# Performance work log

Measured on AMD Instinct MI355X. Metric: run time of the kernel, lower is better.

The kernel has to match this reference:

```python
import jax, jax.numpy as jnp
import numpy as np

B, T, D = 4, 2048, 1024
C_BIAS = 0.0  # init kwarg c
LN_EPS = 1e-5


def setup_inputs() -> dict:
    key = jax.random.key(0)
    ks = jax.random.split(key, 8)
    s = 1.0 / np.sqrt(D)
    return {
        "x": jax.random.normal(ks[0], (B, T, D), dtype=jnp.float32),
        "l": jax.random.randint(ks[1], (B,), 1, T + 1),  # lengths in [1, T]
        "Wq": jax.random.normal(ks[2], (D, D), dtype=jnp.float32) * s,
        "Wk": jax.random.normal(ks[3], (D, D), dtype=jnp.float32) * s,
        "Wv": jax.random.normal(ks[4], (D, D), dtype=jnp.float32) * s,
        "Wo": jax.random.normal(ks[5], (D, D), dtype=jnp.float32) * s,
        "bo": jnp.zeros((D,), dtype=jnp.float32),
        "gamma": jnp.ones((D,), dtype=jnp.float32),
        "beta": jnp.zeros((D,), dtype=jnp.float32),
    }


def reference(x, l, Wq, Wk, Wv, Wo, bo, gamma, beta):
    # LayerNorm over last dim
    mu = jnp.mean(x, axis=-1, keepdims=True)
    var = jnp.mean(jnp.square(x - mu), axis=-1, keepdims=True)
    x_norm = (x - mu) * jax.lax.rsqrt(var + LN_EPS) * gamma + beta

    # QKV projections (torch Linear: y = x @ W.T, no bias)
    q = jnp.einsum("btd,ed->bte", x_norm, Wq)
    k = jnp.einsum("btd,ed->bte", x_norm, Wk)
    v = jnp.einsum("btd,ed->bte", x_norm, Wv)

    scale = 1.0 / jnp.sqrt(jnp.float32(D))
    scores = C_BIAS + jnp.einsum("bid,bjd->bij", q, k) * scale  # [B,T,T]

    # Mask is applied along the ROW (dim 1) axis, and softmax is over dim 1
    # (faithful to the original: mask.unsqueeze(2) + Softmax(dim=1)).
    valid_rows = jnp.arange(T)[None, :] < l[:, None]  # [B,T]
    scores = jnp.where(valid_rows[:, :, None], scores, -jnp.inf)
    attn = jax.nn.softmax(scores, axis=1)  # normalize over rows

    y = x + jnp.einsum("bij,bjd->bid", attn, v)
    out = jax.nn.relu(jnp.einsum("btd,ed->bte", y, Wo) + bo)
    return out
```

## Files before the change

kernel.cpp:

```cpp
#include <hip/hip_runtime.h>
#include <hip/hip_fp16.h>

typedef unsigned short u16;
typedef __attribute__((ext_vector_type(8))) short bf16x8;
typedef __attribute__((ext_vector_type(4))) float f32x4;

#define T_SEQ 2048
#define DIM 1024
#define NB 4
#define NCH 8

__device__ __forceinline__ u16 f2bf(float f) {
  union { float f; unsigned u; } c; c.f = f;
  unsigned r = c.u + 0x7fffu + ((c.u >> 16) & 1u);
  return (u16)(r >> 16);
}

__device__ __forceinline__ void gload_lds16(const void* g, void* l) {
  __builtin_amdgcn_global_load_lds((const __attribute__((address_space(1))) void*)g,
                                   (__attribute__((address_space(3))) void*)l, 16, 0, 0);
}

#define SBAR() asm volatile("s_barrier" ::: "memory")
#define WVL(n) asm volatile("s_waitcnt vmcnt(" n ") lgkmcnt(0)" ::: "memory")

__global__ __launch_bounds__(256) void ln_kernel(const float* __restrict__ x,
                                                 const float* __restrict__ gamma,
                                                 const float* __restrict__ beta,
                                                 u16* __restrict__ xn) {
  const int row = blockIdx.x;
  const int tid = threadIdx.x;
  const float4 v = *(const float4*)(x + (size_t)row * DIM + tid * 4);
  float s  = v.x + v.y + v.z + v.w;
  float ss = v.x * v.x + v.y * v.y + v.z * v.z + v.w * v.w;
#pragma unroll
  for (int o = 32; o > 0; o >>= 1) { s += __shfl_down(s, o); ss += __shfl_down(ss, o); }
  __shared__ float rs[4], rss[4];
  const int wid = tid >> 6, lane = tid & 63;
  if (lane == 0) { rs[wid] = s; rss[wid] = ss; }
  __syncthreads();
  s  = rs[0] + rs[1] + rs[2] + rs[3];
  ss = rss[0] + rss[1] + rss[2] + rss[3];
  const float mu = s * (1.f / DIM);
  const float var = ss * (1.f / DIM) - mu * mu;
  const float rstd = rsqrtf(var + 1e-5f);
  const float4 g  = *(const float4*)(gamma + tid * 4);
  const float4 be = *(const float4*)(beta + tid * 4);
  ushort4 o;
  o.x = f2bf((v.x - mu) * rstd * g.x + be.x);
  o.y = f2bf((v.y - mu) * rstd * g.y + be.y);
  o.z = f2bf((v.z - mu) * rstd * g.z + be.z);
  o.w = f2bf((v.w - mu) * rstd * g.w + be.w);
  *(ushort4*)(xn + (size_t)row * DIM + tid * 4) = o;
}

__global__ __launch_bounds__(256) void wcvt4(const float* __restrict__ wq,
                                             const float* __restrict__ wk,
                                             const float* __restrict__ wv,
                                             const float* __restrict__ wo,
                                             u16* __restrict__ dqk,
                                             u16* __restrict__ dv,
                                             u16* __restrict__ dw) {
  const int sel = blockIdx.x >> 10;
  const size_t t = (size_t)(blockIdx.x & 1023) * 256 + threadIdx.x;
  const float* w = (sel == 0) ? wq : (sel == 1) ? wk : (sel == 2) ? wv : wo;
  u16* d = (sel == 0) ? dqk : (sel == 1) ? (dqk + 1048576) : (sel == 2) ? dv : dw;
  const float4 v = *(const float4*)(w + t * 4);
  ushort4 u; u.x = f2bf(v.x); u.y = f2bf(v.y); u.z = f2bf(v.z); u.w = f2bf(v.w);
  *(ushort4*)(d + t * 4) = u;
}

template <int EPI, int BM, int MSK>
__global__ __launch_bounds__(512, 2) void gemm_bt(
    const u16* __restrict__ A, const u16* __restrict__ B, void* __restrict__ Cv,
    int K, int lda, int ldb, int ldc,
    long sA, long sB, long sC,
    const float* __restrict__ aux, long sAux, float scale,
    const int* __restrict__ lptr, float* __restrict__ mpQ, float* __restrict__ zpQ) {
  constexpr int MI = BM / 32;
  __shared__ __align__(16) u16 As[4][BM * 32];
  __shared__ __align__(16) u16 Bs[4][256 * 32];
  const int bz = blockIdx.z;
  const u16* Ab = A + (size_t)bz * sA;
  const u16* Bb = B + (size_t)bz * sB;

  const int nb = gridDim.x * gridDim.y;
  int bid = blockIdx.y * gridDim.x + blockIdx.x;
  bid = (bid & 7) * (nb >> 3) + (bid >> 3);
  const int gx = gridDim.x;
  const int tileN = (bid % gx) * 256;
  const int tileM = (bid / gx) * BM;

  const int t = threadIdx.x;

  if constexpr (MSK == 1) {
    if (tileM >= lptr[bz]) return;
  }
  if constexpr (MSK == 3) {
    if (((tileM & (T_SEQ - 1)) >= lptr[tileM >> 11]) && tileN < DIM) return;
  }
  if constexpr (MSK == 2) {
    if (tileM >= lptr[bz]) {
      const float* xb = aux + (size_t)bz * sAux;
      u16* yo = (u16*)Cv + (size_t)bz * sC;
      for (int e = t; e < (BM * 256) / 8; e += 512) {
        const int row = tileM + (e >> 5);
        const int col = tileN + ((e & 31) << 3);
        const float4 v0 = *(const float4*)(xb + (size_t)row * ldc + col);
        const float4 v1 = *(const float4*)(xb + (size_t)row * ldc + col + 4);
        ushort4 o0; o0.x = f2bf(v0.x); o0.y = f2bf(v0.y); o0.z = f2bf(v0.z); o0.w = f2bf(v0.w);
        ushort4 o1; o1.x = f2bf(v1.x); o1.y = f2bf(v1.y); o1.z = f2bf(v1.z); o1.w = f2bf(v1.w);
        *(ushort4*)(yo + (size_t)row * ldc + col) = o0;
        *(ushort4*)(yo + (size_t)row * ldc + col + 4) = o1;
      }
      return;
    }
  }

  const int lane = t & 63;
  const int wid = t >> 6;
  const int wm = wid >> 2, wn = wid & 3;

  const int srow = t >> 2;
  const int qsw = (((t & 3) ^ (srow & 3) ^ ((srow >> 2) & 3))) * 8;
  const size_t aoff0 = (size_t)(tileM + srow) * lda + qsw;
  const size_t aoff1 = (size_t)(tileM + 128 + srow) * lda + qsw;
  const size_t boff0 = (size_t)(tileN + srow) * ldb + qsw;
  const size_t boff1 = (size_t)(tileN + 128 + srow) * ldb + qsw;

  const int frow = lane & 15;
  const int kg = lane >> 4;
  const int ckk = ((kg ^ (lane & 3) ^ ((lane >> 2) & 3))) * 8;

  f32x4 acc[MI][4] = {};
  const int NT = K >> 5;

#pragma unroll
  for (int p = 0; p < 3; ++p) {
    const size_t kp = (size_t)p << 5;
    gload_lds16(Ab + aoff0 + kp, &As[p][t * 8]);
    gload_lds16(Bb + boff0 + kp, &Bs[p][t * 8]);
    if constexpr (BM == 256) gload_lds16(Ab + aoff1 + kp, &As[p][4096 + t * 8]);
    gload_lds16(Bb + boff1 + kp, &Bs[p][4096 + t * 8]);
  }
  if constexpr (BM == 256) { asm volatile("s_waitcnt vmcnt(8)" ::: "memory"); }
  else                     { asm volatile("s_waitcnt vmcnt(6)" ::: "memory"); }
  SBAR();

  for (int tau = 0; tau < NT; ++tau) {
    const int cur = tau & 3;
    const int tgt = (tau + 3) & 3;
    const bool st = (tau + 3 < NT);
    const size_t k0 = (size_t)(tau + 3) << 5;

    bf16x8 af[4], bf[4];
#pragma unroll
    for (int j = 0; j < 4; ++j)
      bf[j] = *(const bf16x8*)&Bs[cur][(wn * 64 + j * 16 + frow) * 32 + ckk];
#pragma unroll
    for (int i = 0; i < 4; ++i)
      af[i] = *(const bf16x8*)&As[cur][(wm * (BM / 2) + i * 16 + frow) * 32 + ckk];
    if (st) {
      gload_lds16(Ab + aoff0 + k0, &As[tgt][t * 8]);
      gload_lds16(Bb + boff0 + k0, &Bs[tgt][t * 8]);
      if constexpr (BM == 128) gload_lds16(Bb + boff1 + k0, &Bs[tgt][4096 + t * 8]);
    }
    if constexpr (BM == 128) {
      if (tau < NT - 3) WVL("6"); else if (tau == NT - 3) WVL("3"); else WVL("0");
    }
    SBAR();
    __builtin_amdgcn_s_setprio(1);
#pragma unroll
    for (int i = 0; i < 4; ++i)
#pragma unroll
      for (int j = 0; j < 4; ++j)
        acc[i][j] = __builtin_amdgcn_mfma_f32_16x16x32_bf16(af[i], bf[j], acc[i][j], 0, 0, 0);
    __builtin_amdgcn_s_setprio(0);

    if constexpr (BM == 256) {
      bf16x8 af2[4];
#pragma unroll
      for (int i = 0; i < 4; ++i)
        af2[i] = *(const bf16x8*)&As[cur][(wm * 128 + (4 + i) * 16 + frow) * 32 + ckk];
      if (st) {
        gload_lds16(Ab + aoff1 + k0, &As[tgt][4096 + t * 8]);
        gload_lds16(Bb + boff1 + k0, &Bs[tgt][4096 + t * 8]);
      }
      if (tau < NT - 3) WVL("8"); else if (tau == NT - 3) WVL("4"); else WVL("0");
      SBAR();
      __builtin_amdgcn_s_setprio(1);
#pragma unroll
      for (int i = 0; i < 4; ++i)
#pragma unroll
        for (int j = 0; j < 4; ++j)
          acc[4 + i][j] = __builtin_amdgcn_mfma_f32_16x16x32_bf16(af2[i], bf[j], acc[4 + i][j], 0, 0, 0);
      __builtin_amdgcn_s_setprio(0);
    }
  }

  const int r0 = tileM + wm * (BM / 2) + (kg << 2);
  const int c0 = tileN + wn * 64 + frow;
#pragma unroll
  for (int i = 0; i < MI; ++i)
#pragma unroll
    for (int j = 0; j < 4; ++j)
#pragma unroll
      for (int r = 0; r < 4; ++r) {
        const int row = r0 + i * 16 + r, col = c0 + j * 16;
        const size_t idx = (size_t)row * ldc + col;
        float v = acc[i][j][r];
        if constexpr (EPI == 0) {
          ((u16*)Cv + (size_t)bz * sC)[idx] = f2bf(v);
        } else if constexpr (EPI == 1) {
          ((__half*)Cv + (size_t)bz * sC)[idx] = __float2half(v * scale);
        } else if constexpr (EPI == 2) {
          v += (aux + (size_t)bz * sAux)[idx];
          ((u16*)Cv + (size_t)bz * sC)[idx] = f2bf(v);
        } else {
          v += aux[col];
          ((float*)Cv + (size_t)bz * sC)[idx] = fmaxf(v, 0.f);
        }
      }

  if constexpr (EPI == 1) {
    const int L = lptr[bz];
    __shared__ float2 red[2][4][4][16];
    float Ms[4], Zs[4];
#pragma unroll
    for (int j = 0; j < 4; ++j) {
      float mj = -3e38f;
#pragma unroll
      for (int i = 0; i < MI; ++i)
#pragma unroll
        for (int r = 0; r < 4; ++r) {
          const int row = r0 + i * 16 + r;
          if (row < L) mj = fmaxf(mj, acc[i][j][r] * scale);
        }
      mj = fmaxf(mj, __shfl_xor(mj, 16, 64));
      mj = fmaxf(mj, __shfl_xor(mj, 32, 64));
      float zj = 0.f;
#pragma unroll
      for (int i = 0; i < MI; ++i)
#pragma unroll
        for (int r = 0; r < 4; ++r) {
          const int row = r0 + i * 16 + r;
          if (row < L) zj += __expf(acc[i][j][r] * scale - mj);
        }
      zj += __shfl_xor(zj, 16, 64);
      zj += __shfl_xor(zj, 32, 64);
      Ms[j] = mj; Zs[j] = zj;
    }
    if (lane < 16) {
#pragma unroll
      for (int j = 0; j < 4; ++j) red[wm][wn][j][frow] = make_float2(Ms[j], Zs[j]);
    }
    __syncthreads();
    if (wm == 0 && lane < 16) {
#pragma unroll
      for (int j = 0; j < 4; ++j) {
        const float2 a = red[0][wn][j][frow];
        const float2 b = red[1][wn][j][frow];
        const float M = fmaxf(a.x, b.x);
        const float Z = a.y * __expf(a.x - M) + b.y * __expf(b.x - M);
        const int col = tileN + wn * 64 + j * 16 + frow;
        const size_t o = ((size_t)(tileM >> 8) * NB + bz) * T_SEQ + col;
        mpQ[o] = M; zpQ[o] = Z;
      }
    }
  }
}

__global__ __launch_bounds__(256) void colreduce_comb(const float* __restrict__ mp,
                                                      const float* __restrict__ zp,
                                                      const int* __restrict__ l,
                                                      float* __restrict__ m,
                                                      float* __restrict__ rz) {
  const int b = blockIdx.y;
  const int j = blockIdx.x * 256 + threadIdx.x;
  const int L = l[b];
  float M = -3e38f, Z = 0.f;
  for (int c = 0; c < NCH && (c << 8) < L; ++c) {
    const size_t o = ((size_t)c * NB + b) * T_SEQ + j;
    const float mc = mp[o], zc = zp[o];
    const float nm = fmaxf(M, mc);
    Z = Z * __expf(M - nm) + zc * __expf(mc - nm);
    M = nm;
  }
  m[b * T_SEQ + j] = M;
  rz[b * T_SEQ + j] = 1.f / Z;
}

__global__ __launch_bounds__(256) void pbuild(const __half* __restrict__ S,
                                              const int* __restrict__ l,
                                              const float* __restrict__ m,
                                              const float* __restrict__ rz,
                                              u16* __restrict__ P) {
  const int b = blockIdx.x >> 11;
  const int i = blockIdx.x & (T_SEQ - 1);
  const int L = l[b];
  if (i >= ((L + 127) & ~127)) return;
  const int j0 = threadIdx.x * 8;
  const size_t off = ((size_t)blockIdx.x << 11) + j0;
  ushort4 o0, o1;
  if (i < L) {
    const __half* sp = S + off;
    const float* mp = m + b * T_SEQ + j0;
    const float* zp = rz + b * T_SEQ + j0;
    u16 tmp[8];
#pragma unroll
    for (int t = 0; t < 8; ++t)
      tmp[t] = f2bf(__expf(__half2float(sp[t]) - mp[t]) * zp[t]);
    o0 = make_ushort4(tmp[0], tmp[1], tmp[2], tmp[3]);
    o1 = make_ushort4(tmp[4], tmp[5], tmp[6], tmp[7]);
  } else {
    o0 = make_ushort4(0, 0, 0, 0);
    o1 = make_ushort4(0, 0, 0, 0);
  }
  *(ushort4*)(P + off) = o0;
  *(ushort4*)(P + off + 4) = o1;
}

extern "C" void kernel_launch(void* const* d_in, const int* in_sizes, int n_in,
                              void* d_out, int out_size, void* d_ws, size_t ws_size,
                              hipStream_t stream) {
  (void)in_sizes; (void)n_in; (void)out_size; (void)ws_size;
  const float* x     = (const float*)d_in[0];
  const int*   l     = (const int*)d_in[1];
  const float* Wq    = (const float*)d_in[2];
  const float* Wk    = (const float*)d_in[3];
  const float* Wv    = (const float*)d_in[4];
  const float* Wo    = (const float*)d_in[5];
  const float* bo    = (const float*)d_in[6];
  const float* gamma = (const float*)d_in[7];
  const float* beta  = (const float*)d_in[8];

  char* ws = (char*)d_ws;
  const size_t MiB = 1024 * 1024;
  u16* xn   = (u16*)(ws);
  u16* wqkb = (u16*)(ws + 16 * MiB);
  u16* wvb  = (u16*)(ws + 20 * MiB);
  u16* wob  = (u16*)(ws + 22 * MiB);
  u16* QKb  = (u16*)(ws + 24 * MiB);
  u16* Vt   = (u16*)(ws + 56 * MiB);
  float* mpart = (float*)(ws + 20 * MiB);
  float* zpart = (float*)(ws + 20 * MiB + 512 * 1024);
  float* mb  = (float*)(ws + 72 * MiB);
  float* rzb = (float*)(ws + 72 * MiB + 32 * 1024);
  u16* Pb = QKb;
  u16* yb = xn;
  __half* S = (__half*)d_out;
  float* outp = (float*)d_out;

  const long TD = (long)T_SEQ * DIM, TT = (long)T_SEQ * T_SEQ;
  const long TQK = (long)T_SEQ * 2048;

  ln_kernel<<<NB * T_SEQ, 256, 0, stream>>>(x, gamma, beta, xn);
  wcvt4<<<4096, 256, 0, stream>>>(Wq, Wk, Wv, Wo, wqkb, wvb, wob);

  gemm_bt<0, 256, 3><<<dim3(8, 32, 1), 512, 0, stream>>>(
      xn, wqkb, QKb, DIM, DIM, DIM, 2048, 0, 0, 0, nullptr, 0, 0.f,
      l, nullptr, nullptr);
  gemm_bt<0, 128, 0><<<dim3(32, 8, 1), 512, 0, stream>>>(
      wvb, xn, Vt, DIM, DIM, DIM, 8192, 0, 0, 0, nullptr, 0, 0.f,
      nullptr, nullptr, nullptr);
  gemm_bt<1, 256, 1><<<dim3(8, 8, NB), 512, 0, stream>>>(
      QKb, QKb + 1024, S, DIM, 2048, 2048, T_SEQ, TQK, TQK, TT, nullptr, 0, 0.03125f,
      l, mpart, zpart);
  colreduce_comb<<<dim3(T_SEQ / 256, NB), 256, 0, stream>>>(mpart, zpart, l, mb, rzb);
  pbuild<<<NB * T_SEQ, 256, 0, stream>>>(S, l, mb, rzb, Pb);
  gemm_bt<2, 128, 2><<<dim3(4, 16, NB), 512, 0, stream>>>(
      Pb, Vt, yb, T_SEQ, T_SEQ, 8192, DIM, TT, 2048, TD, x, TD, 0.f,
      l, nullptr, nullptr);
  gemm_bt<3, 128, 0><<<dim3(4, 64, 1), 512, 0, stream>>>(
      yb, wob, outp, DIM, DIM, DIM, DIM, 0, 0, 0, bo, 0, 0.f,
      nullptr, nullptr, nullptr);
}
```

Measured before the change: 208.4 us.

## Add 256x256 GEMM kernel with K=64 double-buffered, finer-grained staged pipeline

Adds a dedicated 256x256-tile GEMM kernel (gemm8) for the QK projection and the QK^T score GEMM. It stages K in 64-wide steps across two double-buffered halves and interleaves half-tile LDS loads, global-to-LDS prefetches and MFMA blocks with barriers between them. The aim is to hide memory latency better than the previous 4-stage, 32-wide scheme. The remaining GEMMs keep a simplified BM=128-only kernel. It adds more barriers per step and a more fragile hand-counted vmcnt schedule.

```diff
diff --git a/kernel.cpp b/kernel.cpp
--- a/kernel.cpp
+++ b/kernel.cpp
@@ -23,6 +23,7 @@
 
 #define SBAR() asm volatile("s_barrier" ::: "memory")
 #define WVL(n) asm volatile("s_waitcnt vmcnt(" n ") lgkmcnt(0)" ::: "memory")
+#define VMC(n) asm volatile("s_waitcnt vmcnt(" n ")" ::: "memory")
 
 __global__ __launch_bounds__(256) void ln_kernel(const float* __restrict__ x,
                                                  const float* __restrict__ gamma,
@@ -70,16 +71,14 @@
   *(ushort4*)(d + t * 4) = u;
 }
 
-template <int EPI, int BM, int MSK>
-__global__ __launch_bounds__(512, 2) void gemm_bt(
+template <int EPI, int MSK>
+__global__ __launch_bounds__(512, 2) void gemm8(
     const u16* __restrict__ A, const u16* __restrict__ B, void* __restrict__ Cv,
     int K, int lda, int ldb, int ldc,
-    long sA, long sB, long sC,
-    const float* __restrict__ aux, long sAux, float scale,
+    long sA, long sB, long sC, float scale,
     const int* __restrict__ lptr, float* __restrict__ mpQ, float* __restrict__ zpQ) {
-  constexpr int MI = BM / 32;
-  __shared__ __align__(16) u16 As[4][BM * 32];
-  __shared__ __align__(16) u16 Bs[4][256 * 32];
+  __shared__ __align__(16) u16 As[2][2][8192];
+  __shared__ __align__(16) u16 Bs[2][2][8192];
   const int bz = blockIdx.z;
   const u16* Ab = A + (size_t)bz * sA;
   const u16* Bb = B + (size_t)bz * sB;
@@ -89,9 +88,7 @@
   bid = (bid & 7) * (nb >> 3) + (bid >> 3);
   const int gx = gridDim.x;
   const int tileN = (bid % gx) * 256;
-  const int tileM = (bid / gx) * BM;
-
-  const int t = threadIdx.x;
+  const int tileM = (bid / gx) * 256;
 
   if constexpr (MSK == 1) {
     if (tileM >= lptr[bz]) return;
@@ -99,11 +96,181 @@
   if constexpr (MSK == 3) {
     if (((tileM & (T_SEQ - 1)) >= lptr[tileM >> 11]) && tileN < DIM) return;
   }
+
+  const int t = threadIdx.x;
+  const int lane = t & 63;
+  const int wid = t >> 6;
+  const int wm = wid >> 2, wn = wid & 3;
+
+  const int srow = wid * 32 + (lane >> 2);
+  const int schk = ((t & 3) ^ (srow & 3) ^ ((srow >> 2) & 3)) * 8;
+  const size_t aof = (size_t)(tileM + srow) * lda + schk;
+  const size_t bof = (size_t)(tileN + srow) * ldb + schk;
+  const size_t a16 = 16 * (size_t)lda, b16 = 16 * (size_t)ldb;
+  const int dst0 = wid * 1024 + lane * 8;
+
+  const int frow = lane & 15, kg = lane >> 4;
+  const int rsw = (kg ^ (frow & 3) ^ ((frow >> 2) & 3)) * 8;
+  const int arow = wm * 128 + frow;
+  const int brow = wn * 64 + frow;
+
+#define STG_A(bf, kk, tg) do { \
+    const size_t _s = aof + (size_t)(tg) * 64 + (kk) * 32; \
+    gload_lds16(Ab + _s, &As[bf][kk][dst0]); \
+    gload_lds16(Ab + _s + a16, &As[bf][kk][dst0 + 512]); } while (0)
+#define STG_B(bf, kk, tg) do { \
+    const size_t _s = bof + (size_t)(tg) * 64 + (kk) * 32; \
+    gload_lds16(Bb + _s, &Bs[bf][kk][dst0]); \
+    gload_lds16(Bb + _s + b16, &Bs[bf][kk][dst0 + 512]); } while (0)
+#define LDA4(bf, kk, h, AF) do { \
+    _Pragma("unroll") for (int _i = 0; _i < 4; ++_i) \
+      AF[_i] = *(const bf16x8*)&As[bf][kk][(arow + (h) * 64 + _i * 16) * 32 + rsw]; } while (0)
+#define LDB4(bf, kk, BF) do { \
+    _Pragma("unroll") for (int _j = 0; _j < 4; ++_j) \
+      BF[_j] = *(const bf16x8*)&Bs[bf][kk][(brow + _j * 16) * 32 + rsw]; } while (0)
+#define MFM(h, AF, BF) do { __builtin_amdgcn_s_setprio(1); \
+    _Pragma("unroll") for (int _i = 0; _i < 4; ++_i) \
+      _Pragma("unroll") for (int _j = 0; _j < 4; ++_j) \
+        acc[(h) * 4 + _i][_j] = __builtin_amdgcn_mfma_f32_16x16x32_bf16( \
+            AF[_i], BF[_j], acc[(h) * 4 + _i][_j], 0, 0, 0); \
+    __builtin_amdgcn_s_setprio(0); } while (0)
+
+  f32x4 acc[8][4] = {};
+  const int NT = K >> 6;
+
+  STG_B(0, 0, 0); STG_A(0, 0, 0);
+  STG_B(0, 1, 0); STG_A(0, 1, 0);
+  STG_B(1, 0, 1); STG_A(1, 0, 1);
+  VMC("4");
+  SBAR();
+
+  for (int tt = 0; tt < NT; tt += 2) {
+    const bool st = (tt + 2 < NT);
+    bf16x8 af[4], bq0[4], bq1[4];
+    LDA4(0, 0, 0, af); LDB4(0, 0, bq0);
+    STG_B(1, 1, tt + 1);
+    SBAR(); MFM(0, af, bq0);
+    LDA4(0, 0, 1, af);
+    STG_A(1, 1, tt + 1);
+    SBAR(); MFM(1, af, bq0);
+    LDA4(0, 1, 0, af); LDB4(0, 1, bq1);
+    if (st) STG_B(0, 0, tt + 2);
+    SBAR(); MFM(0, af, bq1);
+    LDA4(0, 1, 1, af);
+    if (st) { STG_A(0, 0, tt + 2); VMC("4"); } else { VMC("0"); }
+    SBAR(); MFM(1, af, bq1);
+    LDA4(1, 0, 0, af); LDB4(1, 0, bq0);
+    if (st) STG_B(0, 1, tt + 2);
+    SBAR(); MFM(0, af, bq0);
+    LDA4(1, 0, 1, af);
+    if (st) STG_A(0, 1, tt + 2);
+    SBAR(); MFM(1, af, bq0);
+    LDA4(1, 1, 0, af); LDB4(1, 1, bq1);
+    if (st) STG_B(1, 0, tt + 3);
+    SBAR(); MFM(0, af, bq1);
+    LDA4(1, 1, 1, af);
+    if (st) { STG_A(1, 0, tt + 3); VMC("2"); } else { VMC("0"); }
+    SBAR(); MFM(1, af, bq1);
+  }
+#undef STG_A
+#undef STG_B
+#undef LDA4
+#undef LDB4
+#undef MFM
+
+  const int r0 = tileM + wm * 128 + (kg << 2);
+  const int c0 = tileN + wn * 64 + frow;
+#pragma unroll
+  for (int i = 0; i < 8; ++i)
+#pragma unroll
+    for (int j = 0; j < 4; ++j)
+#pragma unroll
+      for (int r = 0; r < 4; ++r) {
+        const int row = r0 + i * 16 + r, col = c0 + j * 16;
+        const size_t idx = (size_t)row * ldc + col;
+        const float v = acc[i][j][r];
+        if constexpr (EPI == 0) {
+          ((u16*)Cv + (size_t)bz * sC)[idx] = f2bf(v);
+        } else {
+          ((__half*)Cv + (size_t)bz * sC)[idx] = __float2half(v * scale);
+        }
+      }
+
+  if constexpr (EPI == 1) {
+    const int L = lptr[bz];
+    __shared__ float2 red[2][4][4][16];
+    float Ms[4], Zs[4];
+#pragma unroll
+    for (int j = 0; j < 4; ++j) {
+      float mj = -3e38f;
+#pragma unroll
+      for (int i = 0; i < 8; ++i)
+#pragma unroll
+        for (int r = 0; r < 4; ++r) {
+          const int row = r0 + i * 16 + r;
+          if (row < L) mj = fmaxf(mj, acc[i][j][r] * scale);
+        }
+      mj = fmaxf(mj, __shfl_xor(mj, 16, 64));
+      mj = fmaxf(mj, __shfl_xor(mj, 32, 64));
+      float zj = 0.f;
+#pragma unroll
+      for (int i = 0; i < 8; ++i)
+#pragma unroll
+        for (int r = 0; r < 4; ++r) {
+          const int row = r0 + i * 16 + r;
+          if (row < L) zj += __expf(acc[i][j][r] * scale - mj);
+        }
+      zj += __shfl_xor(zj, 16, 64);
+      zj += __shfl_xor(zj, 32, 64);
+      Ms[j] = mj; Zs[j] = zj;
+    }
+    if (lane < 16) {
+#pragma unroll
+      for (int j = 0; j < 4; ++j) red[wm][wn][j][frow] = make_float2(Ms[j], Zs[j]);
+    }
+    __syncthreads();
+    if (wm == 0 && lane < 16) {
+#pragma unroll
+      for (int j = 0; j < 4; ++j) {
+        const float2 a = red[0][wn][j][frow];
+        const float2 b = red[1][wn][j][frow];
+        const float M = fmaxf(a.x, b.x);
+        const float Z = a.y * __expf(a.x - M) + b.y * __expf(b.x - M);
+        const int col = tileN + wn * 64 + j * 16 + frow;
+        const size_t o = ((size_t)(tileM >> 8) * NB + bz) * T_SEQ + col;
+        mpQ[o] = M; zpQ[o] = Z;
+      }
+    }
+  }
+}
+
+template <int EPI, int MSK>
+__global__ __launch_bounds__(512, 2) void gemm_bt(
+    const u16* __restrict__ A, const u16* __restrict__ B, void* __restrict__ Cv,
+    int K, int lda, int ldb, int ldc,
+    long sA, long sB, long sC,
+    const float* __restrict__ aux, long sAux,
+    const int* __restrict__ lptr) {
+  __shared__ __align__(16) u16 As[4][128 * 32];
+  __shared__ __align__(16) u16 Bs[4][256 * 32];
+  const int bz = blockIdx.z;
+  const u16* Ab = A + (size_t)bz * sA;
+  const u16* Bb = B + (size_t)bz * sB;
+
+  const int nb = gridDim.x * gridDim.y;
+  int bid = blockIdx.y * gridDim.x + blockIdx.x;
+  bid = (bid & 7) * (nb >> 3) + (bid >> 3);
+  const int gx = gridDim.x;
+  const int tileN = (bid % gx) * 256;
+  const int tileM = (bid / gx) * 128;
+
+  const int t = threadIdx.x;
+
   if constexpr (MSK == 2) {
     if (tileM >= lptr[bz]) {
       const float* xb = aux + (size_t)bz * sAux;
       u16* yo = (u16*)Cv + (size_t)bz * sC;
-      for (int e = t; e < (BM * 256) / 8; e += 512) {
+      for (int e = t; e < (128 * 256) / 8; e += 512) {
         const int row = tileM + (e >> 5);
         const int col = tileN + ((e & 31) << 3);
         const float4 v0 = *(const float4*)(xb + (size_t)row * ldc + col);
@@ -124,7 +291,6 @@
   const int srow = t >> 2;
   const int qsw = (((t & 3) ^ (srow & 3) ^ ((srow >> 2) & 3))) * 8;
   const size_t aoff0 = (size_t)(tileM + srow) * lda + qsw;
-  const size_t aoff1 = (size_t)(tileM + 128 + srow) * lda + qsw;
   const size_t boff0 = (size_t)(tileN + srow) * ldb + qsw;
   const size_t boff1 = (size_t)(tileN + 128 + srow) * ldb + qsw;
 
@@ -132,7 +298,7 @@
   const int kg = lane >> 4;
   const int ckk = ((kg ^ (lane & 3) ^ ((lane >> 2) & 3))) * 8;
 
-  f32x4 acc[MI][4] = {};
+  f32x4 acc[4][4] = {};
   const int NT = K >> 5;
 
 #pragma unroll
@@ -140,11 +306,9 @@
     const size_t kp = (size_t)p << 5;
     gload_lds16(Ab + aoff0 + kp, &As[p][t * 8]);
     gload_lds16(Bb + boff0 + kp, &Bs[p][t * 8]);
-    if constexpr (BM == 256) gload_lds16(Ab + aoff1 + kp, &As[p][4096 + t * 8]);
     gload_lds16(Bb + boff1 + kp, &Bs[p][4096 + t * 8]);
   }
-  if constexpr (BM == 256) { asm volatile("s_waitcnt vmcnt(8)" ::: "memory"); }
-  else                     { asm volatile("s_waitcnt vmcnt(6)" ::: "memory"); }
+  VMC("6");
   SBAR();
 
   for (int tau = 0; tau < NT; ++tau) {
@@ -159,15 +323,13 @@
       bf[j] = *(const bf16x8*)&Bs[cur][(wn * 64 + j * 16 + frow) * 32 + ckk];
 #pragma unroll
     for (int i = 0; i < 4; ++i)
-      af[i] = *(const bf16x8*)&As[cur][(wm * (BM / 2) + i * 16 + frow) * 32 + ckk];
+      af[i] = *(const bf16x8*)&As[cur][(wm * 64 + i * 16 + frow) * 32 + ckk];
     if (st) {
       gload_lds16(Ab + aoff0 + k0, &As[tgt][t * 8]);
       gload_lds16(Bb + boff0 + k0, &Bs[tgt][t * 8]);
-      if constexpr (BM == 128) gload_lds16(Bb + boff1 + k0, &Bs[tgt][4096 + t * 8]);
+      gload_lds16(Bb + boff1 + k0, &Bs[tgt][4096 + t * 8]);
     }
-    if constexpr (BM == 128) {
-      if (tau < NT - 3) WVL("6"); else if (tau == NT - 3) WVL("3"); else WVL("0");
-    }
+    if (tau < NT - 3) WVL("6"); else if (tau == NT - 3) WVL("3"); else WVL("0");
     SBAR();
     __builtin_amdgcn_s_setprio(1);
 #pragma unroll
@@ -176,32 +338,12 @@
       for (int j = 0; j < 4; ++j)
         acc[i][j] = __builtin_amdgcn_mfma_f32_16x16x32_bf16(af[i], bf[j], acc[i][j], 0, 0, 0);
     __builtin_amdgcn_s_setprio(0);
-
-    if constexpr (BM == 256) {
-      bf16x8 af2[4];
-#pragma unroll
-      for (int i = 0; i < 4; ++i)
-        af2[i] = *(const bf16x8*)&As[cur][(wm * 128 + (4 + i) * 16 + frow) * 32 + ckk];
-      if (st) {
-        gload_lds16(Ab + aoff1 + k0, &As[tgt][4096 + t * 8]);
-        gload_lds16(Bb + boff1 + k0, &Bs[tgt][4096 + t * 8]);
-      }
-      if (tau < NT - 3) WVL("8"); else if (tau == NT - 3) WVL("4"); else WVL("0");
-      SBAR();
-      __builtin_amdgcn_s_setprio(1);
-#pragma unroll
-      for (int i = 0; i < 4; ++i)
-#pragma unroll
-        for (int j = 0; j < 4; ++j)
-          acc[4 + i][j] = __builtin_amdgcn_mfma_f32_16x16x32_bf16(af2[i], bf[j], acc[4 + i][j], 0, 0, 0);
-      __builtin_amdgcn_s_setprio(0);
-    }
-  }
-
-  const int r0 = tileM + wm * (BM / 2) + (kg << 2);
+  }
+
+  const int r0 = tileM + wm * 64 + (kg << 2);
   const int c0 = tileN + wn * 64 + frow;
 #pragma unroll
-  for (int i = 0; i < MI; ++i)
+  for (int i = 0; i < 4; ++i)
 #pragma unroll
     for (int j = 0; j < 4; ++j)
 #pragma unroll
@@ -211,8 +353,6 @@
         float v = acc[i][j][r];
         if constexpr (EPI == 0) {
           ((u16*)Cv + (size_t)bz * sC)[idx] = f2bf(v);
-        } else if constexpr (EPI == 1) {
-          ((__half*)Cv + (size_t)bz * sC)[idx] = __float2half(v * scale);
         } else if constexpr (EPI == 2) {
           v += (aux + (size_t)bz * sAux)[idx];
           ((u16*)Cv + (size_t)bz * sC)[idx] = f2bf(v);
@@ -221,53 +361,6 @@
           ((float*)Cv + (size_t)bz * sC)[idx] = fmaxf(v, 0.f);
         }
       }
-
-  if constexpr (EPI == 1) {
-    const int L = lptr[bz];
-    __shared__ float2 red[2][4][4][16];
-    float Ms[4], Zs[4];
-#pragma unroll
-    for (int j = 0; j < 4; ++j) {
-      float mj = -3e38f;
-#pragma unroll
-      for (int i = 0; i < MI; ++i)
-#pragma unroll
-        for (int r = 0; r < 4; ++r) {
-          const int row = r0 + i * 16 + r;
-          if (row < L) mj = fmaxf(mj, acc[i][j][r] * scale);
-        }
-      mj = fmaxf(mj, __shfl_xor(mj, 16, 64));
-      mj = fmaxf(mj, __shfl_xor(mj, 32, 64));
-      float zj = 0.f;
-#pragma unroll
-      for (int i = 0; i < MI; ++i)
-#pragma unroll
-        for (int r = 0; r < 4; ++r) {
-          const int row = r0 + i * 16 + r;
-          if (row < L) zj += __expf(acc[i][j][r] * scale - mj);
-        }
-      zj += __shfl_xor(zj, 16, 64);
-      zj += __shfl_xor(zj, 32, 64);
-      Ms[j] = mj; Zs[j] = zj;
-    }
-    if (lane < 16) {
-#pragma unroll
-      for (int j = 0; j < 4; ++j) red[wm][wn][j][frow] = make_float2(Ms[j], Zs[j]);
-    }
-    __syncthreads();
-    if (wm == 0 && lane < 16) {
-#pragma unroll
-      for (int j = 0; j < 4; ++j) {
-        const float2 a = red[0][wn][j][frow];
-        const float2 b = red[1][wn][j][frow];
-        const float M = fmaxf(a.x, b.x);
-        const float Z = a.y * __expf(a.x - M) + b.y * __expf(b.x - M);
-        const int col = tileN + wn * 64 + j * 16 + frow;
-        const size_t o = ((size_t)(tileM >> 8) * NB + bz) * T_SEQ + col;
-        mpQ[o] = M; zpQ[o] = Z;
-      }
-    }
-  }
 }
 
 __global__ __launch_bounds__(256) void colreduce_comb(const float* __restrict__ mp,
@@ -308,8 +401,8 @@
     const float* zp = rz + b * T_SEQ + j0;
     u16 tmp[8];
 #pragma unroll
-    for (int t = 0; t < 8; ++t)
-      tmp[t] = f2bf(__expf(__half2float(sp[t]) - mp[t]) * zp[t]);
+    for (int tt = 0; tt < 8; ++tt)
+      tmp[tt] = f2bf(__expf(__half2float(sp[tt]) - mp[tt]) * zp[tt]);
     o0 = make_ushort4(tmp[0], tmp[1], tmp[2], tmp[3]);
     o1 = make_ushort4(tmp[4], tmp[5], tmp[6], tmp[7]);
   } else {
@@ -357,21 +450,17 @@
   ln_kernel<<<NB * T_SEQ, 256, 0, stream>>>(x, gamma, beta, xn);
   wcvt4<<<4096, 256, 0, stream>>>(Wq, Wk, Wv, Wo, wqkb, wvb, wob);
 
-  gemm_bt<0, 256, 3><<<dim3(8, 32, 1), 512, 0, stream>>>(
-      xn, wqkb, QKb, DIM, DIM, DIM, 2048, 0, 0, 0, nullptr, 0, 0.f,
-      l, nullptr, nullptr);
-  gemm_bt<0, 128, 0><<<dim3(32, 8, 1), 512, 0, stream>>>(
-      wvb, xn, Vt, DIM, DIM, DIM, 8192, 0, 0, 0, nullptr, 0, 0.f,
-      nullptr, nullptr, nullptr);
-  gemm_bt<1, 256, 1><<<dim3(8, 8, NB), 512, 0, stream>>>(
-      QKb, QKb + 1024, S, DIM, 2048, 2048, T_SEQ, TQK, TQK, TT, nullptr, 0, 0.03125f,
+  gemm8<0, 3><<<dim3(8, 32, 1), 512, 0, stream>>>(
+      xn, wqkb, QKb, DIM, DIM, DIM, 2048, 0, 0, 0, 0.f, l, nullptr, nullptr);
+  gemm_bt<0, 0><<<dim3(32, 8, 1), 512, 0, stream>>>(
+      wvb, xn, Vt, DIM, DIM, DIM, 8192, 0, 0, 0, nullptr, 0, nullptr);
+  gemm8<1, 1><<<dim3(8, 8, NB), 512, 0, stream>>>(
+      QKb, QKb + 1024, S, DIM, 2048, 2048, T_SEQ, TQK, TQK, TT, 0.03125f,
       l, mpart, zpart);
   colreduce_comb<<<dim3(T_SEQ / 256, NB), 256, 0, stream>>>(mpart, zpart, l, mb, rzb);
   pbuild<<<NB * T_SEQ, 256, 0, stream>>>(S, l, mb, rzb, Pb);
-  gemm_bt<2, 128, 2><<<dim3(4, 16, NB), 512, 0, stream>>>(
-      Pb, Vt, yb, T_SEQ, T_SEQ, 8192, DIM, TT, 2048, TD, x, TD, 0.f,
-      l, nullptr, nullptr);
-  gemm_bt<3, 128, 0><<<dim3(4, 64, 1), 512, 0, stream>>>(
-      yb, wob, outp, DIM, DIM, DIM, DIM, 0, 0, 0, bo, 0, 0.f,
-      nullptr, nullptr, nullptr);
-}
+  gemm_bt<2, 2><<<dim3(4, 16, NB), 512, 0, stream>>>(
+      Pb, Vt, yb, T_SEQ, T_SEQ, 8192, DIM, TT, 2048, TD, x, TD, l);
+  gemm_bt<3, 0><<<dim3(4, 64, 1), 512, 0, stream>>>(
+      yb, wob, outp, DIM, DIM, DIM, DIM, 0, 0, 0, bo, 0, nullptr);
+}
```

Measured after the change: 208.7 us. About the same (+0.1%).

## Replace pipelined 256-wide GEMM with simple 128x128 single-buffer GEMM kernel

Applied to the files above, without the earlier changes.

Swaps the 4-stage software-pipelined GEMM (256x256 or 128x256 tiles, 512 threads, asm waitcnt/barriers) for a simpler 128x128 tile kernel with 256 threads, K-step 64, one LDS buffer and __syncthreads. Grids are doubled and the softmax column-partial chunk count goes from 8 to 16 to match the smaller row tiles. This trades the load/compute overlap and larger tile reuse for higher occupancy, finer masking granularity and less per-block LDS. The loss of prefetch overlap may expose global-load latency.

```diff
diff --git a/kernel.cpp b/kernel.cpp
--- a/kernel.cpp
+++ b/kernel.cpp
@@ -8,7 +8,7 @@
 #define T_SEQ 2048
 #define DIM 1024
 #define NB 4
-#define NCH 8
+#define NCH 16
 
 __device__ __forceinline__ u16 f2bf(float f) {
   union { float f; unsigned u; } c; c.f = f;
@@ -20,9 +20,6 @@
   __builtin_amdgcn_global_load_lds((const __attribute__((address_space(1))) void*)g,
                                    (__attribute__((address_space(3))) void*)l, 16, 0, 0);
 }
-
-#define SBAR() asm volatile("s_barrier" ::: "memory")
-#define WVL(n) asm volatile("s_waitcnt vmcnt(" n ") lgkmcnt(0)" ::: "memory")
 
 __global__ __launch_bounds__(256) void ln_kernel(const float* __restrict__ x,
                                                  const float* __restrict__ gamma,
@@ -70,16 +67,15 @@
   *(ushort4*)(d + t * 4) = u;
 }
 
-template <int EPI, int BM, int MSK>
-__global__ __launch_bounds__(512, 2) void gemm_bt(
+template <int EPI, int MSK>
+__global__ __launch_bounds__(256, 4) void gemm97(
     const u16* __restrict__ A, const u16* __restrict__ B, void* __restrict__ Cv,
     int K, int lda, int ldb, int ldc,
-    long sA, long sB, long sC,
-    const float* __restrict__ aux, long sAux, float scale,
+    long sA, long sB, long sC, float scale,
+    const float* __restrict__ aux, long sAux,
     const int* __restrict__ lptr, float* __restrict__ mpQ, float* __restrict__ zpQ) {
-  constexpr int MI = BM / 32;
-  __shared__ __align__(16) u16 As[4][BM * 32];
-  __shared__ __align__(16) u16 Bs[4][256 * 32];
+  __shared__ __align__(16) u16 As[128 * 64];
+  __shared__ __align__(16) u16 Bs[128 * 64];
   const int bz = blockIdx.z;
   const u16* Ab = A + (size_t)bz * sA;
   const u16* Bb = B + (size_t)bz * sB;
@@ -88,8 +84,8 @@
   int bid = blockIdx.y * gridDim.x + blockIdx.x;
   bid = (bid & 7) * (nb >> 3) + (bid >> 3);
   const int gx = gridDim.x;
-  const int tileN = (bid % gx) * 256;
-  const int tileM = (bid / gx) * BM;
+  const int tileN = (bid % gx) * 128;
+  const int tileM = (bid / gx) * 128;
 
   const int t = threadIdx.x;
 
@@ -103,9 +99,9 @@
     if (tileM >= lptr[bz]) {
       const float* xb = aux + (size_t)bz * sAux;
       u16* yo = (u16*)Cv + (size_t)bz * sC;
-      for (int e = t; e < (BM * 256) / 8; e += 512) {
-        const int row = tileM + (e >> 5);
-        const int col = tileN + ((e & 31) << 3);
+      for (int e = t; e < (128 * 128) / 8; e += 256) {
+        const int row = tileM + (e >> 4);
+        const int col = tileN + ((e & 15) << 3);
         const float4 v0 = *(const float4*)(xb + (size_t)row * ldc + col);
         const float4 v1 = *(const float4*)(xb + (size_t)row * ldc + col + 4);
         ushort4 o0; o0.x = f2bf(v0.x); o0.y = f2bf(v0.y); o0.z = f2bf(v0.z); o0.w = f2bf(v0.w);
@@ -119,89 +115,47 @@
 
   const int lane = t & 63;
   const int wid = t >> 6;
-  const int wm = wid >> 2, wn = wid & 3;
-
-  const int srow = t >> 2;
-  const int qsw = (((t & 3) ^ (srow & 3) ^ ((srow >> 2) & 3))) * 8;
-  const size_t aoff0 = (size_t)(tileM + srow) * lda + qsw;
-  const size_t aoff1 = (size_t)(tileM + 128 + srow) * lda + qsw;
-  const size_t boff0 = (size_t)(tileN + srow) * ldb + qsw;
-  const size_t boff1 = (size_t)(tileN + 128 + srow) * ldb + qsw;
-
-  const int frow = lane & 15;
-  const int kg = lane >> 4;
-  const int ckk = ((kg ^ (lane & 3) ^ ((lane >> 2) & 3))) * 8;
-
-  f32x4 acc[MI][4] = {};
-  const int NT = K >> 5;
-
-#pragma unroll
-  for (int p = 0; p < 3; ++p) {
-    const size_t kp = (size_t)p << 5;
-    gload_lds16(Ab + aoff0 + kp, &As[p][t * 8]);
-    gload_lds16(Bb + boff0 + kp, &Bs[p][t * 8]);
-    if constexpr (BM == 256) gload_lds16(Ab + aoff1 + kp, &As[p][4096 + t * 8]);
-    gload_lds16(Bb + boff1 + kp, &Bs[p][4096 + t * 8]);
-  }
-  if constexpr (BM == 256) { asm volatile("s_waitcnt vmcnt(8)" ::: "memory"); }
-  else                     { asm volatile("s_waitcnt vmcnt(6)" ::: "memory"); }
-  SBAR();
-
-  for (int tau = 0; tau < NT; ++tau) {
-    const int cur = tau & 3;
-    const int tgt = (tau + 3) & 3;
-    const bool st = (tau + 3 < NT);
-    const size_t k0 = (size_t)(tau + 3) << 5;
-
-    bf16x8 af[4], bf[4];
-#pragma unroll
-    for (int j = 0; j < 4; ++j)
-      bf[j] = *(const bf16x8*)&Bs[cur][(wn * 64 + j * 16 + frow) * 32 + ckk];
-#pragma unroll
-    for (int i = 0; i < 4; ++i)
-      af[i] = *(const bf16x8*)&As[cur][(wm * (BM / 2) + i * 16 + frow) * 32 + ckk];
-    if (st) {
-      gload_lds16(Ab + aoff0 + k0, &As[tgt][t * 8]);
-      gload_lds16(Bb + boff0 + k0, &Bs[tgt][t * 8]);
-      if constexpr (BM == 128) gload_lds16(Bb + boff1 + k0, &Bs[tgt][4096 + t * 8]);
-    }
-    if constexpr (BM == 128) {
-      if (tau < NT - 3) WVL("6"); else if (tau == NT - 3) WVL("3"); else WVL("0");
-    }
-    SBAR();
-    __builtin_amdgcn_s_setprio(1);
-#pragma unroll
-    for (int i = 0; i < 4; ++i)
+  const int wm = wid >> 1, wn = wid & 1;
+
+  const int r0s = t >> 3;
+  const int sch = ((t & 7) ^ (r0s & 7)) * 8;
+
+  const int frow = lane & 15, kg = lane >> 4, f7 = lane & 7;
+
+  f32x4 acc[4][4] = {};
+
+  for (int k0 = 0; k0 < K; k0 += 64) {
+    if (k0) __syncthreads();
+#pragma unroll
+    for (int i = 0; i < 4; ++i) {
+      const int e = i * 256 + t;
+      const int row = i * 32 + r0s;
+      gload_lds16(Ab + (size_t)(tileM + row) * lda + k0 + sch, &As[e * 8]);
+      gload_lds16(Bb + (size_t)(tileN + row) * ldb + k0 + sch, &Bs[e * 8]);
+    }
+    __syncthreads();
+#pragma unroll
+    for (int h = 0; h < 2; ++h) {
+      const int cs = (((h * 4 + kg) ^ f7)) * 8;
+      bf16x8 af[4], bf[4];
+#pragma unroll
+      for (int i = 0; i < 4; ++i)
+        af[i] = *(const bf16x8*)&As[(wm * 64 + i * 16 + frow) * 64 + cs];
 #pragma unroll
       for (int j = 0; j < 4; ++j)
-        acc[i][j] = __builtin_amdgcn_mfma_f32_16x16x32_bf16(af[i], bf[j], acc[i][j], 0, 0, 0);
-    __builtin_amdgcn_s_setprio(0);
-
-    if constexpr (BM == 256) {
-      bf16x8 af2[4];
+        bf[j] = *(const bf16x8*)&Bs[(wn * 64 + j * 16 + frow) * 64 + cs];
 #pragma unroll
       for (int i = 0; i < 4; ++i)
-        af2[i] = *(const bf16x8*)&As[cur][(wm * 128 + (4 + i) * 16 + frow) * 32 + ckk];
-      if (st) {
-        gload_lds16(Ab + aoff1 + k0, &As[tgt][4096 + t * 8]);
-        gload_lds16(Bb + boff1 + k0, &Bs[tgt][4096 + t * 8]);
-      }
-      if (tau < NT - 3) WVL("8"); else if (tau == NT - 3) WVL("4"); else WVL("0");
-      SBAR();
-      __builtin_amdgcn_s_setprio(1);
-#pragma unroll
-      for (int i = 0; i < 4; ++i)
 #pragma unroll
         for (int j = 0; j < 4; ++j)
-          acc[4 + i][j] = __builtin_amdgcn_mfma_f32_16x16x32_bf16(af2[i], bf[j], acc[4 + i][j], 0, 0, 0);
-      __builtin_amdgcn_s_setprio(0);
-    }
-  }
-
-  const int r0 = tileM + wm * (BM / 2) + (kg << 2);
+          acc[i][j] = __builtin_amdgcn_mfma_f32_16x16x32_bf16(af[i], bf[j], acc[i][j], 0, 0, 0);
+    }
+  }
+
+  const int r0 = tileM + wm * 64 + (kg << 2);
   const int c0 = tileN + wn * 64 + frow;
 #pragma unroll
-  for (int i = 0; i < MI; ++i)
+  for (int i = 0; i < 4; ++i)
 #pragma unroll
     for (int j = 0; j < 4; ++j)
 #pragma unroll
@@ -224,13 +178,13 @@
 
   if constexpr (EPI == 1) {
     const int L = lptr[bz];
-    __shared__ float2 red[2][4][4][16];
+    __shared__ float2 red[2][2][4][16];
     float Ms[4], Zs[4];
 #pragma unroll
     for (int j = 0; j < 4; ++j) {
       float mj = -3e38f;
 #pragma unroll
-      for (int i = 0; i < MI; ++i)
+      for (int i = 0; i < 4; ++i)
 #pragma unroll
         for (int r = 0; r < 4; ++r) {
           const int row = r0 + i * 16 + r;
@@ -240,7 +194,7 @@
       mj = fmaxf(mj, __shfl_xor(mj, 32, 64));
       float zj = 0.f;
 #pragma unroll
-      for (int i = 0; i < MI; ++i)
+      for (int i = 0; i < 4; ++i)
 #pragma unroll
         for (int r = 0; r < 4; ++r) {
           const int row = r0 + i * 16 + r;
@@ -263,7 +217,7 @@
         const float M = fmaxf(a.x, b.x);
         const float Z = a.y * __expf(a.x - M) + b.y * __expf(b.x - M);
         const int col = tileN + wn * 64 + j * 16 + frow;
-        const size_t o = ((size_t)(tileM >> 8) * NB + bz) * T_SEQ + col;
+        const size_t o = ((size_t)(tileM >> 7) * NB + bz) * T_SEQ + col;
         mpQ[o] = M; zpQ[o] = Z;
       }
     }
@@ -279,7 +233,7 @@
   const int j = blockIdx.x * 256 + threadIdx.x;
   const int L = l[b];
   float M = -3e38f, Z = 0.f;
-  for (int c = 0; c < NCH && (c << 8) < L; ++c) {
+  for (int c = 0; c < NCH && (c << 7) < L; ++c) {
     const size_t o = ((size_t)c * NB + b) * T_SEQ + j;
     const float mc = mp[o], zc = zp[o];
     const float nm = fmaxf(M, mc);
@@ -308,8 +262,8 @@
     const float* zp = rz + b * T_SEQ + j0;
     u16 tmp[8];
 #pragma unroll
-    for (int t = 0; t < 8; ++t)
-      tmp[t] = f2bf(__expf(__half2float(sp[t]) - mp[t]) * zp[t]);
+    for (int tt = 0; tt < 8; ++tt)
+      tmp[tt] = f2bf(__expf(__half2float(sp[tt]) - mp[tt]) * zp[tt]);
     o0 = make_ushort4(tmp[0], tmp[1], tmp[2], tmp[3]);
     o1 = make_ushort4(tmp[4], tmp[5], tmp[6], tmp[7]);
   } else {
@@ -357,21 +311,21 @@
   ln_kernel<<<NB * T_SEQ, 256, 0, stream>>>(x, gamma, beta, xn);
   wcvt4<<<4096, 256, 0, stream>>>(Wq, Wk, Wv, Wo, wqkb, wvb, wob);
 
-  gemm_bt<0, 256, 3><<<dim3(8, 32, 1), 512, 0, stream>>>(
-      xn, wqkb, QKb, DIM, DIM, DIM, 2048, 0, 0, 0, nullptr, 0, 0.f,
+  gemm97<0, 3><<<dim3(16, 64, 1), 256, 0, stream>>>(
+      xn, wqkb, QKb, DIM, DIM, DIM, 2048, 0, 0, 0, 0.f, nullptr, 0,
       l, nullptr, nullptr);
-  gemm_bt<0, 128, 0><<<dim3(32, 8, 1), 512, 0, stream>>>(
-      wvb, xn, Vt, DIM, DIM, DIM, 8192, 0, 0, 0, nullptr, 0, 0.f,
+  gemm97<0, 0><<<dim3(64, 8, 1), 256, 0, stream>>>(
+      wvb, xn, Vt, DIM, DIM, DIM, 8192, 0, 0, 0, 0.f, nullptr, 0,
       nullptr, nullptr, nullptr);
-  gemm_bt<1, 256, 1><<<dim3(8, 8, NB), 512, 0, stream>>>(
-      QKb, QKb + 1024, S, DIM, 2048, 2048, T_SEQ, TQK, TQK, TT, nullptr, 0, 0.03125f,
-      l, mpart, zpart);
+  gemm97<1, 1><<<dim3(16, 16, NB), 256, 0, stream>>>(
+      QKb, QKb + 1024, S, DIM, 2048, 2048, T_SEQ, TQK, TQK, TT, 0.03125f,
+      nullptr, 0, l, mpart, zpart);
   colreduce_comb<<<dim3(T_SEQ / 256, NB), 256, 0, stream>>>(mpart, zpart, l, mb, rzb);
   pbuild<<<NB * T_SEQ, 256, 0, stream>>>(S, l, mb, rzb, Pb);
-  gemm_bt<2, 128, 2><<<dim3(4, 16, NB), 512, 0, stream>>>(
-      Pb, Vt, yb, T_SEQ, T_SEQ, 8192, DIM, TT, 2048, TD, x, TD, 0.f,
+  gemm97<2, 2><<<dim3(8, 16, NB), 256, 0, stream>>>(
+      Pb, Vt, yb, T_SEQ, T_SEQ, 8192, DIM, TT, 2048, TD, 0.f, x, TD,
       l, nullptr, nullptr);
-  gemm_bt<3, 128, 0><<<dim3(4, 64, 1), 512, 0, stream>>>(
-      yb, wob, outp, DIM, DIM, DIM, DIM, 0, 0, 0, bo, 0, 0.f,
+  gemm97<3, 0><<<dim3(8, 64, 1), 256, 0, stream>>>(
+      yb, wob, outp, DIM, DIM, DIM, DIM, 0, 0, 0, 0.f, bo, 0,
       nullptr, nullptr, nullptr);
 }
```

After: 206.8 us. Within noise of the previous version (-0.7%).
